# Performance work log

Hardware: AMD Instinct MI355X
Metric: run time of the kernel (lower is better)

## Reference

```python
import jax, jax.numpy as jnp
import numpy as np

N_NODES = 50000
N_GRAPHS = 64
VOCAB = 100000
D = 256
PAD_IDX = 0


def setup_inputs() -> dict:
    key = jax.random.key(0)
    ks = jax.random.split(key, 8)
    seq = jax.random.randint(ks[0], (N_NODES, 16), 0, VOCAB)
    edge_index = jax.random.randint(ks[1], (2, 800000), 0, N_NODES)
    batch = jnp.sort(jax.random.randint(ks[2], (N_NODES,), 0, N_GRAPHS))
    emb = jax.random.normal(ks[3], (VOCAB, D), dtype=jnp.float32) * 0.02
    emb = emb.at[PAD_IDX].set(0.0)  # padding_idx row is zero
    W0 = jax.random.normal(ks[4], (D, D), dtype=jnp.float32) * (1.0 / np.sqrt(D))
    b0 = jnp.zeros((D,), dtype=jnp.float32)
    W1 = jax.random.normal(ks[5], (D, D), dtype=jnp.float32) * (1.0 / np.sqrt(D))
    b1 = jnp.zeros((D,), dtype=jnp.float32)
    return {"seq": seq, "edge_index": edge_index, "batch": batch,
            "emb": emb, "W0": W0, "b0": b0, "W1": W1, "b1": b1}


def _gcn_layer(x, W, b, src, dst, dis):
    # GCN with self-loops and symmetric normalization.
    h = x @ W + b  # [N, D]
    norm = dis[src] * dis[dst]  # [E]
    agg = jax.ops.segment_sum(h[src] * norm[:, None], dst, num_segments=N_NODES)
    agg = agg + h * (dis * dis)[:, None]  # self-loop contribution
    return agg


def reference(seq, edge_index, batch, emb, W0, b0, W1, b1):
    # statement encoder: embedding lookup + sum over token parts
    x = jnp.sum(emb[seq], axis=1)  # [N, D]
    src, dst = edge_index[0], edge_index[1]
    # degree with self-loops (counted on destination)
    deg = jax.ops.segment_sum(jnp.ones_like(dst, dtype=x.dtype), dst,
                              num_segments=N_NODES) + 1.0
    dis = jax.lax.rsqrt(deg)  # deg^{-1/2}
    h = _gcn_layer(x, W0, b0, src, dst, dis)
    h = jax.nn.relu(h)
    h = _gcn_layer(h, W1, b1, src, dst, dis)
    out = jax.nn.relu(h)
    # global sum pool over graph ids
    pooled = jax.ops.segment_sum(out, batch, num_segments=N_GRAPHS)  # [G, D]
    return pooled
```

## Files before the change

### kernel.cpp

```cpp
#include <hip/hip_runtime.h>
#include <stdint.h>

#define N_NODES 50000
#define N_GRAPHS 64
#define VOCAB 100000
#define DIM 256
#define N_EDGES 800000
#define T_SEQ 16
#define CAP 64
#define FILL_BLOCKS 3125

typedef short bf16x8 __attribute__((ext_vector_type(8)));
typedef unsigned short u16x8 __attribute__((ext_vector_type(8)));
typedef unsigned short u16x4 __attribute__((ext_vector_type(4)));
typedef float f32x4 __attribute__((ext_vector_type(4)));
typedef unsigned short u16;

__device__ __forceinline__ float bf2f(u16 u) {
    union { unsigned int i; float f; } v; v.i = ((unsigned int)u) << 16; return v.f;
}
__device__ __forceinline__ u16 f2bf(float f) {
    union { float f; unsigned int i; } v; v.f = f;
    unsigned int x = v.i;
    return (u16)((x + 0x7fffu + ((x >> 16) & 1u)) >> 16);
}

__global__ __launch_bounds__(256) void prep_kernel(const float* __restrict__ emb,
        u16* __restrict__ emb_bf, const float* __restrict__ W0, u16* __restrict__ WT0,
        const float* __restrict__ W1, u16* __restrict__ WT1,
        int* __restrict__ counts, float* __restrict__ out) {
    int bid = blockIdx.x;
    if (bid < 12500) {
        size_t base = ((size_t)bid * 256 + threadIdx.x) * 8;
        float4 a = *(const float4*)(emb + base);
        float4 b = *(const float4*)(emb + base + 4);
        ushort4 o0, o1;
        o0.x = f2bf(a.x); o0.y = f2bf(a.y); o0.z = f2bf(a.z); o0.w = f2bf(a.w);
        o1.x = f2bf(b.x); o1.y = f2bf(b.y); o1.z = f2bf(b.z); o1.w = f2bf(b.w);
        *(ushort4*)(emb_bf + base) = o0;
        *(ushort4*)(emb_bf + base + 4) = o1;
        if (bid < 196) {
            int i = bid * 256 + threadIdx.x;
            if (i < N_NODES) counts[i] = 0;
        }
        if (bid < 64) out[bid * 256 + threadIdx.x] = 0.f;
    } else {
        __shared__ u16 tile[32][33];
        int b = bid - 12500;
        int which = b >> 6;
        const float* W = which ? W1 : W0;
        u16* WT = which ? WT1 : WT0;
        b &= 63;
        int bx = b & 7, by = b >> 3;
        int tx = threadIdx.x & 31, ty = threadIdx.x >> 5;
#pragma unroll
        for (int r = 0; r < 32; r += 8)
            tile[ty + r][tx] = f2bf(W[(size_t)(by * 32 + ty + r) * DIM + bx * 32 + tx]);
        __syncthreads();
#pragma unroll
        for (int r = 0; r < 32; r += 8)
            WT[(size_t)(bx * 32 + ty + r) * DIM + by * 32 + tx] = tile[tx][ty + r];
    }
}

__global__ __launch_bounds__(256) void encode_fill_kernel(
        const int* __restrict__ seq, const u16* __restrict__ emb,
        u16* __restrict__ x,
        const int* __restrict__ esrc, const int* __restrict__ edst,
        int* __restrict__ counts, int* __restrict__ bucket) {
    int bid = blockIdx.x;
    if (bid < FILL_BLOCKS) {
        int e = bid * 256 + threadIdx.x;
        int d = edst[e];
        int p = atomicAdd(&counts[d], 1);
        if (p < CAP) bucket[(size_t)d * CAP + p] = esrc[e];
        return;
    }
    int nb = bid - FILL_BLOCKS;
    int wave = threadIdx.x >> 6, lane = threadIdx.x & 63;
    int n = nb * 4 + wave;
    int half = lane >> 5, l32 = lane & 31;
    int c = l32 * 8;
    int toks[8];
#pragma unroll
    for (int tt = 0; tt < 8; ++tt)
        toks[tt] = seq[n * T_SEQ + half + 2 * tt];
    u16x8 v[8];
#pragma unroll
    for (int tt = 0; tt < 8; ++tt)
        v[tt] = *(const u16x8*)(emb + (size_t)toks[tt] * DIM + c);
    __builtin_amdgcn_sched_barrier(0);
    float a[8] = {0.f, 0.f, 0.f, 0.f, 0.f, 0.f, 0.f, 0.f};
#pragma unroll
    for (int tt = 0; tt < 8; ++tt)
#pragma unroll
        for (int j = 0; j < 8; ++j) a[j] += bf2f(v[tt][j]);
#pragma unroll
    for (int j = 0; j < 8; ++j) a[j] += __shfl_xor(a[j], 32, 64);
    if (half == 0) {
        u16x8 o;
#pragma unroll
        for (int j = 0; j < 8; ++j) o[j] = f2bf(a[j]);
        *(u16x8*)(x + (size_t)n * DIM + c) = o;
    }
}

__global__ __launch_bounds__(256) void gemm_kernel(const u16* __restrict__ A,
        const u16* __restrict__ WT, const float* __restrict__ bias,
        const int* __restrict__ counts, u16* __restrict__ C, int M) {
    __shared__ __align__(16) uint8_t ldsA[128 * 64];
    __shared__ __align__(16) uint8_t ldsB[128 * 64];
    int tid = threadIdx.x;
    int wave = tid >> 6, lane = tid & 63;
    int quad = lane >> 4, l16 = lane & 15;
    int wm = wave & 1, wn = wave >> 1;
    int bm = blockIdx.y * 128, bn = blockIdx.x * 128;

    f32x4 acc[4][4] = {};

    for (int kt = 0; kt < 8; ++kt) {
        int k0 = kt * 32;
#pragma unroll
        for (int i = 0; i < 2; ++i) {
            int chunk = tid + i * 256;
            int row = chunk >> 2;
            int coff = (chunk & 3) * 16;
            int gr = bm + row; if (gr > M - 1) gr = M - 1;
            uint4 va = *(const uint4*)((const uint8_t*)A + ((size_t)gr * DIM + k0) * 2 + coff);
            *(uint4*)(ldsA + row * 64 + coff) = va;
            uint4 vb = *(const uint4*)((const uint8_t*)WT + ((size_t)(bn + row) * DIM + k0) * 2 + coff);
            *(uint4*)(ldsB + row * 64 + coff) = vb;
        }
        __syncthreads();
        bf16x8 afr[4], bfr[4];
#pragma unroll
        for (int t = 0; t < 4; ++t) {
            afr[t] = *(const bf16x8*)(ldsA + (wm * 64 + t * 16 + l16) * 64 + quad * 16);
            bfr[t] = *(const bf16x8*)(ldsB + (wn * 64 + t * 16 + l16) * 64 + quad * 16);
        }
#pragma unroll
        for (int tm = 0; tm < 4; ++tm)
#pragma unroll
            for (int tn = 0; tn < 4; ++tn)
                acc[tm][tn] = __builtin_amdgcn_mfma_f32_16x16x32_bf16(
                    afr[tm], bfr[tn], acc[tm][tn], 0, 0, 0);
        __syncthreads();
    }

    float bv[4];
#pragma unroll
    for (int tn = 0; tn < 4; ++tn) bv[tn] = bias[bn + wn * 64 + tn * 16 + l16];
#pragma unroll
    for (int tm = 0; tm < 4; ++tm) {
        int row0 = bm + wm * 64 + tm * 16 + quad * 4;
#pragma unroll
        for (int r = 0; r < 4; ++r) {
            int row = row0 + r;
            if (row < M) {
                int cnt = counts[row]; if (cnt > CAP) cnt = CAP;
                float dsc = rsqrtf((float)cnt + 1.0f);
#pragma unroll
                for (int tn = 0; tn < 4; ++tn) {
                    int col = bn + wn * 64 + tn * 16 + l16;
                    C[(size_t)row * DIM + col] = f2bf((acc[tm][tn][r] + bv[tn]) * dsc);
                }
            }
        }
    }
}

__global__ __launch_bounds__(256) void agg_kernel(const u16* __restrict__ h,
        const int* __restrict__ counts, const int* __restrict__ bucket,
        u16* __restrict__ z) {
    int wave = threadIdx.x >> 6, lane = threadIdx.x & 63;
    int n = blockIdx.x * 4 + wave;
    if (n >= N_NODES) return;
    int half = lane >> 5, l32 = lane & 31;
    int c = l32 * 8;
    float a[8];
    if (half == 0) {
        u16x8 v = *(const u16x8*)(h + (size_t)n * DIM + c);
#pragma unroll
        for (int j = 0; j < 8; ++j) a[j] = bf2f(v[j]);
    } else {
#pragma unroll
        for (int j = 0; j < 8; ++j) a[j] = 0.f;
    }
    int cnt = counts[n]; if (cnt > CAP) cnt = CAP;
    const int* bk = bucket + (size_t)n * CAP;
    int e = half;
    for (; e + 14 < cnt; e += 16) {
        int s0 = bk[e];      int s1 = bk[e + 2];
        int s2 = bk[e + 4];  int s3 = bk[e + 6];
        int s4 = bk[e + 8];  int s5 = bk[e + 10];
        int s6 = bk[e + 12]; int s7 = bk[e + 14];
        u16x8 v0 = *(const u16x8*)(h + (size_t)s0 * DIM + c);
        u16x8 v1 = *(const u16x8*)(h + (size_t)s1 * DIM + c);
        u16x8 v2 = *(const u16x8*)(h + (size_t)s2 * DIM + c);
        u16x8 v3 = *(const u16x8*)(h + (size_t)s3 * DIM + c);
        u16x8 v4 = *(const u16x8*)(h + (size_t)s4 * DIM + c);
        u16x8 v5 = *(const u16x8*)(h + (size_t)s5 * DIM + c);
        u16x8 v6 = *(const u16x8*)(h + (size_t)s6 * DIM + c);
        u16x8 v7 = *(const u16x8*)(h + (size_t)s7 * DIM + c);
        __builtin_amdgcn_sched_barrier(0);
#pragma unroll
        for (int j = 0; j < 8; ++j)
            a[j] += ((bf2f(v0[j]) + bf2f(v1[j])) + (bf2f(v2[j]) + bf2f(v3[j]))) +
                    ((bf2f(v4[j]) + bf2f(v5[j])) + (bf2f(v6[j]) + bf2f(v7[j])));
    }
    for (; e + 6 < cnt; e += 8) {
        int s0 = bk[e];
        int s1 = bk[e + 2];
        int s2 = bk[e + 4];
        int s3 = bk[e + 6];
        u16x8 v0 = *(const u16x8*)(h + (size_t)s0 * DIM + c);
        u16x8 v1 = *(const u16x8*)(h + (size_t)s1 * DIM + c);
        u16x8 v2 = *(const u16x8*)(h + (size_t)s2 * DIM + c);
        u16x8 v3 = *(const u16x8*)(h + (size_t)s3 * DIM + c);
#pragma unroll
        for (int j = 0; j < 8; ++j)
            a[j] += bf2f(v0[j]) + bf2f(v1[j]) + bf2f(v2[j]) + bf2f(v3[j]);
    }
    for (; e < cnt; e += 2) {
        int s = bk[e];
        u16x8 v = *(const u16x8*)(h + (size_t)s * DIM + c);
#pragma unroll
        for (int j = 0; j < 8; ++j) a[j] += bf2f(v[j]);
    }
#pragma unroll
    for (int j = 0; j < 8; ++j) a[j] += __shfl_xor(a[j], 32, 64);
    if (half == 0) {
        float dn = rsqrtf((float)cnt + 1.0f);
        u16x8 o;
#pragma unroll
        for (int j = 0; j < 8; ++j) o[j] = f2bf(fmaxf(a[j] * dn, 0.f));
        *(u16x8*)(z + (size_t)n * DIM + c) = o;
    }
}

__global__ __launch_bounds__(256) void pool_kernel(const u16* __restrict__ z,
        const int* __restrict__ batch, float* __restrict__ out) {
    const int NWAVES = 4096;
    const int NPW = (N_NODES + NWAVES - 1) / NWAVES;
    int gw = blockIdx.x * 4 + (threadIdx.x >> 6);
    int lane = threadIdx.x & 63;
    int n0 = gw * NPW;
    if (n0 >= N_NODES) return;
    int n1 = n0 + NPW; if (n1 > N_NODES) n1 = N_NODES;
    int c = lane * 4;
    float a0 = 0.f, a1 = 0.f, a2 = 0.f, a3 = 0.f;
    int gprev = -1;
    for (int n = n0; n < n1; ++n) {
        int g = batch[n];
        if (g != gprev) {
            if (gprev >= 0) {
                float* o = out + (size_t)gprev * DIM + c;
                atomicAdd(o + 0, a0); atomicAdd(o + 1, a1);
                atomicAdd(o + 2, a2); atomicAdd(o + 3, a3);
            }
            a0 = a1 = a2 = a3 = 0.f; gprev = g;
        }
        u16x4 v = *(const u16x4*)(z + (size_t)n * DIM + c);
        a0 += bf2f(v[0]); a1 += bf2f(v[1]); a2 += bf2f(v[2]); a3 += bf2f(v[3]);
    }
    if (gprev >= 0) {
        float* o = out + (size_t)gprev * DIM + c;
        atomicAdd(o + 0, a0); atomicAdd(o + 1, a1);
        atomicAdd(o + 2, a2); atomicAdd(o + 3, a3);
    }
}

extern "C" void kernel_launch(void* const* d_in, const int* in_sizes, int n_in,
                              void* d_out, int out_size, void* d_ws, size_t ws_size,
                              hipStream_t stream) {
    const int*   seq   = (const int*)d_in[0];
    const int*   eidx  = (const int*)d_in[1];
    const int*   batch = (const int*)d_in[2];
    const float* emb   = (const float*)d_in[3];
    const float* W0    = (const float*)d_in[4];
    const float* b0    = (const float*)d_in[5];
    const float* W1    = (const float*)d_in[6];
    const float* b1    = (const float*)d_in[7];
    float* out = (float*)d_out;

    uint8_t* ws = (uint8_t*)d_ws;
    size_t off = 0;
    auto alloc = [&](size_t bytes) -> uint8_t* {
        uint8_t* p = ws + off;
        off += (bytes + 255) & ~(size_t)255;
        return p;
    };
    u16* emb_bf  = (u16*)alloc((size_t)VOCAB * DIM * 2);
    u16* buf0    = (u16*)alloc((size_t)N_NODES * DIM * 2);
    u16* buf1    = (u16*)alloc((size_t)N_NODES * DIM * 2);
    int* bucket  = (int*)alloc((size_t)N_NODES * CAP * 4);
    int* counts  = (int*)alloc((size_t)N_NODES * 4);
    u16* WT0     = (u16*)alloc((size_t)DIM * DIM * 2);
    u16* WT1     = (u16*)alloc((size_t)DIM * DIM * 2);

    const int* esrc = eidx;
    const int* edst = eidx + N_EDGES;

    prep_kernel<<<12500 + 128, 256, 0, stream>>>(emb, emb_bf, W0, WT0, W1, WT1,
                                                 counts, out);
    encode_fill_kernel<<<FILL_BLOCKS + 12500, 256, 0, stream>>>(
        seq, emb_bf, buf0, esrc, edst, counts, bucket);

    dim3 ggrid(2, (N_NODES + 127) / 128);
    gemm_kernel<<<ggrid, 256, 0, stream>>>(buf0, WT0, b0, counts, buf1, N_NODES);
    agg_kernel<<<(N_NODES + 3) / 4, 256, 0, stream>>>(buf1, counts, bucket, buf0);
    gemm_kernel<<<ggrid, 256, 0, stream>>>(buf0, WT1, b1, counts, buf1, N_NODES);
    agg_kernel<<<(N_NODES + 3) / 4, 256, 0, stream>>>(buf1, counts, bucket, buf0);

    pool_kernel<<<1024, 256, 0, stream>>>(buf0, batch, out);
}
```

Baseline: 451.3 us.

## Use u16 neighbor buckets, direct-to-LDS GEMM loads, and split encode/fill kernels

Neighbor bucket indices are stored as 16-bit values, since node ids stay below 65536. This halves bucket write and read traffic in the fill and aggregation kernels. The GEMM tile staging now uses global_load_lds with 16-byte transfers straight into shared memory, replacing the path through registers. The fused encode/fill kernel is split into two separate launches, which removes the block-index branching but gives up any overlap between the atomic fill work and the embedding gather.

```diff
diff --git a/kernel.cpp b/kernel.cpp
--- a/kernel.cpp
+++ b/kernel.cpp
@@ -8,7 +8,6 @@
 #define N_EDGES 800000
 #define T_SEQ 16
 #define CAP 64
-#define FILL_BLOCKS 3125
 
 typedef short bf16x8 __attribute__((ext_vector_type(8)));
 typedef unsigned short u16x8 __attribute__((ext_vector_type(8)));
@@ -23,6 +22,12 @@
     union { float f; unsigned int i; } v; v.f = f;
     unsigned int x = v.i;
     return (u16)((x + 0x7fffu + ((x >> 16) & 1u)) >> 16);
+}
+
+__device__ __forceinline__ void gload_lds16(const void* g, void* l) {
+    __builtin_amdgcn_global_load_lds(
+        (const __attribute__((address_space(1))) uint32_t*)g,
+        (__attribute__((address_space(3))) uint32_t*)l, 16, 0, 0);
 }
 
 __global__ __launch_bounds__(256) void prep_kernel(const float* __restrict__ emb,
@@ -63,22 +68,21 @@
     }
 }
 
-__global__ __launch_bounds__(256) void encode_fill_kernel(
-        const int* __restrict__ seq, const u16* __restrict__ emb,
-        u16* __restrict__ x,
-        const int* __restrict__ esrc, const int* __restrict__ edst,
-        int* __restrict__ counts, int* __restrict__ bucket) {
-    int bid = blockIdx.x;
-    if (bid < FILL_BLOCKS) {
-        int e = bid * 256 + threadIdx.x;
-        int d = edst[e];
+__global__ void fill_kernel(const int* __restrict__ src, const int* __restrict__ dst,
+        int* __restrict__ counts, u16* __restrict__ bucket) {
+    int e = blockIdx.x * 256 + threadIdx.x;
+    if (e < N_EDGES) {
+        int d = dst[e];
         int p = atomicAdd(&counts[d], 1);
-        if (p < CAP) bucket[(size_t)d * CAP + p] = esrc[e];
-        return;
-    }
-    int nb = bid - FILL_BLOCKS;
+        if (p < CAP) bucket[(size_t)d * CAP + p] = (u16)src[e];
+    }
+}
+
+__global__ __launch_bounds__(256) void encode_kernel(const int* __restrict__ seq,
+        const u16* __restrict__ emb, u16* __restrict__ x) {
     int wave = threadIdx.x >> 6, lane = threadIdx.x & 63;
-    int n = nb * 4 + wave;
+    int n = blockIdx.x * 4 + wave;
+    if (n >= N_NODES) return;
     int half = lane >> 5, l32 = lane & 31;
     int c = l32 * 8;
     int toks[8];
@@ -116,20 +120,23 @@
     int wm = wave & 1, wn = wave >> 1;
     int bm = blockIdx.y * 128, bn = blockIdx.x * 128;
 
+    int srow = wave * 32 + (lane >> 2);
+    int sbyte = (lane & 3) * 16;
+    uint8_t* dstA = ldsA + wave * 2048;
+    uint8_t* dstB = ldsB + wave * 2048;
+
     f32x4 acc[4][4] = {};
 
     for (int kt = 0; kt < 8; ++kt) {
-        int k0 = kt * 32;
-#pragma unroll
-        for (int i = 0; i < 2; ++i) {
-            int chunk = tid + i * 256;
-            int row = chunk >> 2;
-            int coff = (chunk & 3) * 16;
-            int gr = bm + row; if (gr > M - 1) gr = M - 1;
-            uint4 va = *(const uint4*)((const uint8_t*)A + ((size_t)gr * DIM + k0) * 2 + coff);
-            *(uint4*)(ldsA + row * 64 + coff) = va;
-            uint4 vb = *(const uint4*)((const uint8_t*)WT + ((size_t)(bn + row) * DIM + k0) * 2 + coff);
-            *(uint4*)(ldsB + row * 64 + coff) = vb;
+        int k0b = kt * 64;
+#pragma unroll
+        for (int q = 0; q < 2; ++q) {
+            int gr = bm + srow + q * 16; if (gr > M - 1) gr = M - 1;
+            gload_lds16((const uint8_t*)A + (size_t)gr * (DIM * 2) + k0b + sbyte,
+                        dstA + q * 1024);
+            int gbr = bn + srow + q * 16;
+            gload_lds16((const uint8_t*)WT + (size_t)gbr * (DIM * 2) + k0b + sbyte,
+                        dstB + q * 1024);
         }
         __syncthreads();
         bf16x8 afr[4], bfr[4];
@@ -170,7 +177,7 @@
 }
 
 __global__ __launch_bounds__(256) void agg_kernel(const u16* __restrict__ h,
-        const int* __restrict__ counts, const int* __restrict__ bucket,
+        const int* __restrict__ counts, const u16* __restrict__ bucket,
         u16* __restrict__ z) {
     int wave = threadIdx.x >> 6, lane = threadIdx.x & 63;
     int n = blockIdx.x * 4 + wave;
@@ -187,7 +194,7 @@
         for (int j = 0; j < 8; ++j) a[j] = 0.f;
     }
     int cnt = counts[n]; if (cnt > CAP) cnt = CAP;
-    const int* bk = bucket + (size_t)n * CAP;
+    const u16* bk = bucket + (size_t)n * CAP;
     int e = half;
     for (; e + 14 < cnt; e += 16) {
         int s0 = bk[e];      int s1 = bk[e + 2];
@@ -293,7 +300,7 @@
     u16* emb_bf  = (u16*)alloc((size_t)VOCAB * DIM * 2);
     u16* buf0    = (u16*)alloc((size_t)N_NODES * DIM * 2);
     u16* buf1    = (u16*)alloc((size_t)N_NODES * DIM * 2);
-    int* bucket  = (int*)alloc((size_t)N_NODES * CAP * 4);
+    u16* bucket  = (u16*)alloc((size_t)N_NODES * CAP * 2);
     int* counts  = (int*)alloc((size_t)N_NODES * 4);
     u16* WT0     = (u16*)alloc((size_t)DIM * DIM * 2);
     u16* WT1     = (u16*)alloc((size_t)DIM * DIM * 2);
@@ -303,8 +310,8 @@
 
     prep_kernel<<<12500 + 128, 256, 0, stream>>>(emb, emb_bf, W0, WT0, W1, WT1,
                                                  counts, out);
-    encode_fill_kernel<<<FILL_BLOCKS + 12500, 256, 0, stream>>>(
-        seq, emb_bf, buf0, esrc, edst, counts, bucket);
+    fill_kernel<<<(N_EDGES + 255) / 256, 256, 0, stream>>>(esrc, edst, counts, bucket);
+    encode_kernel<<<(N_NODES + 3) / 4, 256, 0, stream>>>(seq, emb_bf, buf0);
 
     dim3 ggrid(2, (N_NODES + 127) / 128);
     gemm_kernel<<<ggrid, 256, 0, stream>>>(buf0, WT0, b0, counts, buf1, N_NODES);
```

After: 442.0 us. 1.02x faster.
